# Kernel tuning notes

Measured on AMD Instinct MI355X. Metric: run time of the kernel, lower is better.

The kernel has to match this reference:

```python
import jax, jax.numpy as jnp
import numpy as np

B, T, D, H = 64, 512, 1024, 1024

def setup_inputs() -> dict:
    key = jax.random.key(0)
    k1, k2, k3, k4 = jax.random.split(key, 4)
    inputs = jax.random.normal(k1, (B, T, D), dtype=jnp.float32)
    lengths = jax.random.randint(k2, (B,), 1, T + 1, dtype=jnp.int32)
    init_c = jnp.zeros((B, H), dtype=jnp.float32)
    init_h = jnp.zeros((B, H), dtype=jnp.float32)
    # LSTMCell params: input kernel (no bias), hidden kernel + bias, gates [i,f,g,o]
    Wi = jax.random.normal(k3, (D, 4 * H), dtype=jnp.float32) / np.sqrt(D)
    Wh = jax.random.normal(k4, (H, 4 * H), dtype=jnp.float32) / np.sqrt(H)
    b = jnp.zeros((4 * H,), dtype=jnp.float32)
    return {"inputs": inputs, "lengths": lengths, "init_c": init_c,
            "init_h": init_h, "Wi": Wi, "Wh": Wh, "b": b}

def reference(inputs, lengths, init_c, init_h, Wi, Wh, b):
    # Precompute the input-side projection for all timesteps (same math as
    # per-step dense_i in flax LSTMCell, just batched).
    x_proj = jnp.einsum('btd,dg->btg', inputs, Wi) + b  # [B, T, 4H]

    def step(carry, x):
        c, h = carry
        z = x + h @ Wh  # [B, 4H]
        i, f, g, o = jnp.split(z, 4, axis=-1)
        i = jax.nn.sigmoid(i)
        f = jax.nn.sigmoid(f)
        g = jnp.tanh(g)
        o = jax.nn.sigmoid(o)
        new_c = f * c + i * g
        new_h = o * jnp.tanh(new_c)
        return (new_c, new_h), (new_c, new_h)

    _, (cs, hs) = jax.lax.scan(step, (init_c, init_h),
                               jnp.swapaxes(x_proj, 0, 1))  # [T, B, H] each
    outputs = jnp.swapaxes(hs, 0, 1)       # [B, T, H]
    cell_cs = jnp.swapaxes(cs, 0, 1)       # [B, T, H]
    idx = jnp.arange(inputs.shape[0])
    final_c = cell_cs[idx, lengths - 1]    # [B, H]
    final_h = outputs[idx, lengths - 1]    # [B, H]
    return outputs, final_c, final_h
```

## Files before the change

### kernel.cpp

```cpp
#include <hip/hip_runtime.h>

#define B_ 64
#define T_ 512
#define D_ 1024
#define H_ 1024

typedef _Float16 half8 __attribute__((ext_vector_type(8)));
typedef float floatx16 __attribute__((ext_vector_type(16)));

__device__ __forceinline__ float sigm(float x)   { return 1.f / (1.f + __expf(-x)); }
__device__ __forceinline__ float tanh_f(float x) { return 1.f - 2.f / (1.f + __expf(2.f * x)); }

__global__ void k_prep_x(const float* __restrict__ x, _Float16* __restrict__ xf) {
  int i = blockIdx.x * blockDim.x + threadIdx.x;
  const float4* p = (const float4*)x + (size_t)i * 2;
  float4 a = p[0], b = p[1];
  half8 v;
  v[0]=(_Float16)a.x; v[1]=(_Float16)a.y; v[2]=(_Float16)a.z; v[3]=(_Float16)a.w;
  v[4]=(_Float16)b.x; v[5]=(_Float16)b.y; v[6]=(_Float16)b.z; v[7]=(_Float16)b.w;
  ((half8*)xf)[i] = v;
}

__global__ void k_prep_misc(const float* __restrict__ init_h,
                            _Float16* __restrict__ hb1, int* __restrict__ flags) {
  int i = blockIdx.x * blockDim.x + threadIdx.x;
  hb1[i] = (_Float16)init_h[i];
  if (i < 4096) flags[i] = 0;
}

template <bool XF16>
__launch_bounds__(256, 1)
__global__ void k_lstm(const float* __restrict__ x32, const _Float16* __restrict__ xf,
                       const int* __restrict__ lengths, const float* __restrict__ init_c,
                       const float* __restrict__ Wi, const float* __restrict__ Wh,
                       const float* __restrict__ bias,
                       _Float16* __restrict__ hb0, _Float16* __restrict__ hb1,
                       int* __restrict__ flags,
                       float* __restrict__ out, float* __restrict__ finc,
                       float* __restrict__ finh)
{
  __shared__ _Float16 slab[32768];
  __shared__ _Float16 hlds[32][1028];
  __shared__ float red[4][32][40];

  const int w    = blockIdx.x;
  const int bh   = w >> 7;
  const int jc   = w & 127;
  const int t    = threadIdx.x;
  const int wave = t >> 6;
  const int lane = t & 63;
  const int m    = lane & 31;
  const int kh   = lane >> 5;

  const int gate = m >> 3;
  const int col  = gate * H_ + jc * 8 + (m & 7);

  for (int kbb = 0; kbb < 16; ++kbb) {
    const int kb = kbb * 4 + wave;
    const int kc = kb * 16 + kh * 8;
    half8 v;
    #pragma unroll
    for (int j = 0; j < 8; ++j)
      v[j] = (_Float16)Wh[(size_t)(kc + j) * 4096 + col];
    *(half8*)&slab[kb * 512 + lane * 8] = v;
  }

  half8 wia[16];
  #pragma unroll
  for (int i = 0; i < 16; ++i) {
    const int kc = (wave * 16 + i) * 16 + kh * 8;
    half8 v;
    #pragma unroll
    for (int j = 0; j < 8; ++j)
      v[j] = (_Float16)Wi[(size_t)(kc + j) * 4096 + col];
    wia[i] = v;
  }

  const int bl = t >> 3, jj = t & 7;
  const int bG = bh * 32 + bl;
  const int jG = jc * 8 + jj;
  float c = init_c[bG * H_ + jG];
  const int len = lengths[bG];
  const float bz0 = bias[0 * H_ + jG];
  const float bz1 = bias[1 * H_ + jG];
  const float bz2 = bias[2 * H_ + jG];
  const float bz3 = bias[3 * H_ + jG];

  const int bA = bh * 32 + m;
  const _Float16* xbase   = XF16 ? (xf + (size_t)bA * T_ * D_ + kh * 8) : (const _Float16*)0;
  const float*    xbase32 = x32 + (size_t)bA * T_ * D_ + kh * 8;

  int* myflag_w = flags + (w << 4);
  int* pollflag = flags + ((bh * 128 + wave * 32 + m) << 4);

  __syncthreads();

  half8 xa[16];
  if (XF16) {
    const _Float16* xs = xbase;
    #pragma unroll
    for (int i = 0; i < 16; ++i)
      xa[i] = *(const half8*)(xs + (wave * 16 + i) * 16);
  }

  for (int s = 0; s < T_; ++s) {
    if (lane < 32) {
      int spin = 0;
      while (__hip_atomic_load(pollflag, __ATOMIC_RELAXED, __HIP_MEMORY_SCOPE_AGENT) < s) {
        __builtin_amdgcn_s_sleep(1);
        if (++spin > (1 << 22)) break;
      }
    }

    const _Float16* hsrc = (s & 1) ? hb0 : hb1;
    const unsigned long long* hq =
        (const unsigned long long*)hsrc + (size_t)bh * 8192;
    unsigned long long q[32];
    #pragma unroll
    for (int r = 0; r < 32; ++r)
      q[r] = __hip_atomic_load(hq + r * 256 + wave * 64 + lane,
                               __ATOMIC_RELAXED, __HIP_MEMORY_SCOPE_AGENT);

    floatx16 C;
    #pragma unroll
    for (int r = 0; r < 16; ++r) C[r] = 0.f;
    if (XF16) {
      #pragma unroll
      for (int i = 0; i < 16; ++i)
        C = __builtin_amdgcn_mfma_f32_32x32x16_f16(xa[i], wia[i], C, 0, 0, 0);
    } else {
      const float* xs = xbase32 + (size_t)s * D_;
      #pragma unroll
      for (int i = 0; i < 16; ++i) {
        const float4* p = (const float4*)(xs + (wave * 16 + i) * 16);
        float4 u0 = p[0], u1 = p[1];
        half8 v;
        v[0]=(_Float16)u0.x; v[1]=(_Float16)u0.y; v[2]=(_Float16)u0.z; v[3]=(_Float16)u0.w;
        v[4]=(_Float16)u1.x; v[5]=(_Float16)u1.y; v[6]=(_Float16)u1.z; v[7]=(_Float16)u1.w;
        C = __builtin_amdgcn_mfma_f32_32x32x16_f16(v, wia[i], C, 0, 0, 0);
      }
    }

    #pragma unroll
    for (int r = 0; r < 32; ++r)
      *(unsigned long long*)&hlds[r][wave * 256 + lane * 4] = q[r];

    #pragma unroll
    for (int i = 0; i < 16; ++i) {
      const half8 av = *(const half8*)&hlds[m][wave * 256 + i * 16 + kh * 8];
      const half8 bf = *(const half8*)&slab[(wave * 16 + i) * 512 + lane * 8];
      C = __builtin_amdgcn_mfma_f32_32x32x16_f16(av, bf, C, 0, 0, 0);
    }

    #pragma unroll
    for (int r = 0; r < 16; ++r) {
      const int row = (r & 3) + 8 * (r >> 2) + 4 * kh;
      red[wave][row][m] = C[r];
    }
    __syncthreads();

    const float z0 = red[0][bl][jj]      + red[1][bl][jj]      + red[2][bl][jj]      + red[3][bl][jj]      + bz0;
    const float z1 = red[0][bl][8 + jj]  + red[1][bl][8 + jj]  + red[2][bl][8 + jj]  + red[3][bl][8 + jj]  + bz1;
    const float z2 = red[0][bl][16 + jj] + red[1][bl][16 + jj] + red[2][bl][16 + jj] + red[3][bl][16 + jj] + bz2;
    const float z3 = red[0][bl][24 + jj] + red[1][bl][24 + jj] + red[2][bl][24 + jj] + red[3][bl][24 + jj] + bz3;

    const float ig = sigm(z0);
    const float fg = sigm(z1);
    const float gg = tanh_f(z2);
    const float og = sigm(z3);
    c = fg * c + ig * gg;
    const float hv = og * tanh_f(c);

    {
      const float hv_other = __shfl_xor(hv, 1);
      if (!(t & 1)) {
        union { _Float16 h2[2]; unsigned u; } pk;
        pk.h2[0] = (_Float16)hv;
        pk.h2[1] = (_Float16)hv_other;
        _Float16* hdst = (s & 1) ? hb1 : hb0;
        __hip_atomic_store((unsigned*)(hdst + (size_t)bG * H_ + jG), pk.u,
                           __ATOMIC_RELAXED, __HIP_MEMORY_SCOPE_AGENT);
      }
    }

    __syncthreads();
    if (t == 0)
      __hip_atomic_store(myflag_w, s + 1, __ATOMIC_RELAXED, __HIP_MEMORY_SCOPE_AGENT);

    __builtin_nontemporal_store(hv, &out[((size_t)bG * T_ + s) * H_ + jG]);
    if (s == len - 1) {
      __builtin_nontemporal_store(c,  &finc[bG * H_ + jG]);
      __builtin_nontemporal_store(hv, &finh[bG * H_ + jG]);
    }

    if (XF16 && (s + 1 < T_)) {
      const _Float16* xs = xbase + (size_t)(s + 1) * D_;
      #pragma unroll
      for (int i = 0; i < 16; ++i)
        xa[i] = *(const half8*)(xs + (wave * 16 + i) * 16);
    }
  }
}

extern "C" void kernel_launch(void* const* d_in, const int* in_sizes, int n_in,
                              void* d_out, int out_size, void* d_ws, size_t ws_size,
                              hipStream_t stream) {
  const float* x32    = (const float*)d_in[0];
  const int*   lens   = (const int*)  d_in[1];
  const float* init_c = (const float*)d_in[2];
  const float* init_h = (const float*)d_in[3];
  const float* Wi     = (const float*)d_in[4];
  const float* Wh     = (const float*)d_in[5];
  const float* bias   = (const float*)d_in[6];

  float* out   = (float*)d_out;
  float* fin_c = out + (size_t)B_ * T_ * H_;
  float* fin_h = fin_c + (size_t)B_ * H_;

  char* ws = (char*)d_ws;
  int*       flags = (int*)ws;
  _Float16*  hb0   = (_Float16*)(ws + 16384);
  _Float16*  hb1   = hb0 + (size_t)B_ * H_;
  _Float16*  xf16  = (_Float16*)(ws + (1u << 20));

  const size_t need_big = (1u << 20) + sizeof(_Float16) * (size_t)B_ * T_ * D_;

  k_prep_misc<<<256, 256, 0, stream>>>(init_h, hb1, flags);
  if (ws_size >= need_big) {
    k_prep_x<<<16384, 256, 0, stream>>>(x32, xf16);
    k_lstm<true><<<256, 256, 0, stream>>>(x32, xf16, lens, init_c, Wi, Wh, bias,
                                          hb0, hb1, flags, out, fin_c, fin_h);
  } else {
    k_lstm<false><<<256, 256, 0, stream>>>(x32, xf16, lens, init_c, Wi, Wh, bias,
                                           hb0, hb1, flags, out, fin_c, fin_h);
  }
}
```

Measured before the change: 2.471 ms.

## Replace per-step flag polling with epoch bits embedded in fp16 hidden data

```diff
diff --git a/kernel.cpp b/kernel.cpp
--- a/kernel.cpp
+++ b/kernel.cpp
@@ -22,10 +22,13 @@
 }
 
 __global__ void k_prep_misc(const float* __restrict__ init_h,
-                            _Float16* __restrict__ hb1, int* __restrict__ flags) {
+                            unsigned short* __restrict__ hb0,
+                            unsigned short* __restrict__ hb1) {
   int i = blockIdx.x * blockDim.x + threadIdx.x;
-  hb1[i] = (_Float16)init_h[i];
-  if (i < 4096) flags[i] = 0;
+  union { _Float16 h; unsigned short u; } cv;
+  cv.h = (_Float16)init_h[i];
+  hb1[i] = (unsigned short)~cv.u;
+  hb0[i] = 0xFFFFu;
 }
 
 template <bool XF16>
@@ -35,7 +38,6 @@
                        const float* __restrict__ Wi, const float* __restrict__ Wh,
                        const float* __restrict__ bias,
                        _Float16* __restrict__ hb0, _Float16* __restrict__ hb1,
-                       int* __restrict__ flags,
                        float* __restrict__ out, float* __restrict__ finc,
                        float* __restrict__ finh)
 {
@@ -90,9 +92,6 @@
   const _Float16* xbase   = XF16 ? (xf + (size_t)bA * T_ * D_ + kh * 8) : (const _Float16*)0;
   const float*    xbase32 = x32 + (size_t)bA * T_ * D_ + kh * 8;
 
-  int* myflag_w = flags + (w << 4);
-  int* pollflag = flags + ((bh * 128 + wave * 32 + m) << 4);
-
   __syncthreads();
 
   half8 xa[16];
@@ -104,17 +103,11 @@
   }
 
   for (int s = 0; s < T_; ++s) {
-    if (lane < 32) {
-      int spin = 0;
-      while (__hip_atomic_load(pollflag, __ATOMIC_RELAXED, __HIP_MEMORY_SCOPE_AGENT) < s) {
-        __builtin_amdgcn_s_sleep(1);
-        if (++spin > (1 << 22)) break;
-      }
-    }
+    const int eg = (s == 0) ? 1 : (((s - 1) >> 1) & 1);
 
     const _Float16* hsrc = (s & 1) ? hb0 : hb1;
-    const unsigned long long* hq =
-        (const unsigned long long*)hsrc + (size_t)bh * 8192;
+    unsigned long long* hq =
+        (unsigned long long*)hsrc + (size_t)bh * 8192;
     unsigned long long q[32];
     #pragma unroll
     for (int r = 0; r < 32; ++r)
@@ -141,6 +134,28 @@
       }
     }
 
+    {
+      int spin = 0;
+      while (true) {
+        bool all = true;
+        #pragma unroll
+        for (int r = 0; r < 32; ++r) {
+          if ((int)((q[r] >> 14) & 1ull) != eg) {
+            q[r] = __hip_atomic_load(hq + r * 256 + wave * 64 + lane,
+                                     __ATOMIC_RELAXED, __HIP_MEMORY_SCOPE_AGENT);
+            all = false;
+          }
+        }
+        if (all) break;
+        __builtin_amdgcn_s_sleep(1);
+        if (++spin > (1 << 21)) break;
+      }
+      if (eg) {
+        #pragma unroll
+        for (int r = 0; r < 32; ++r) q[r] = ~q[r];
+      }
+    }
+
     #pragma unroll
     for (int r = 0; r < 32; ++r)
       *(unsigned long long*)&hlds[r][wave * 256 + lane * 4] = q[r];
@@ -151,6 +166,8 @@
       const half8 bf = *(const half8*)&slab[(wave * 16 + i) * 512 + lane * 8];
       C = __builtin_amdgcn_mfma_f32_32x32x16_f16(av, bf, C, 0, 0, 0);
     }
+
+    __syncthreads();
 
     #pragma unroll
     for (int r = 0; r < 16; ++r) {
@@ -172,20 +189,20 @@
     const float hv = og * tanh_f(c);
 
     {
-      const float hv_other = __shfl_xor(hv, 1);
-      if (!(t & 1)) {
-        union { _Float16 h2[2]; unsigned u; } pk;
-        pk.h2[0] = (_Float16)hv;
-        pk.h2[1] = (_Float16)hv_other;
+      const int g = (s >> 1) & 1;
+      union { _Float16 h2[2]; unsigned u; } pk;
+      pk.h2[0] = (_Float16)hv;
+      pk.h2[1] = (_Float16)__shfl_xor(hv, 1);
+      const unsigned other = __shfl_xor(pk.u, 2);
+      if ((t & 3) == 0) {
+        unsigned long long qq = (unsigned long long)pk.u
+                              | ((unsigned long long)other << 32);
+        if (g) qq = ~qq;
         _Float16* hdst = (s & 1) ? hb1 : hb0;
-        __hip_atomic_store((unsigned*)(hdst + (size_t)bG * H_ + jG), pk.u,
+        __hip_atomic_store((unsigned long long*)(hdst + (size_t)bG * H_ + jG), qq,
                            __ATOMIC_RELAXED, __HIP_MEMORY_SCOPE_AGENT);
       }
     }
-
-    __syncthreads();
-    if (t == 0)
-      __hip_atomic_store(myflag_w, s + 1, __ATOMIC_RELAXED, __HIP_MEMORY_SCOPE_AGENT);
 
     __builtin_nontemporal_store(hv, &out[((size_t)bG * T_ + s) * H_ + jG]);
     if (s == len - 1) {
@@ -218,20 +235,20 @@
   float* fin_h = fin_c + (size_t)B_ * H_;
 
   char* ws = (char*)d_ws;
-  int*       flags = (int*)ws;
   _Float16*  hb0   = (_Float16*)(ws + 16384);
   _Float16*  hb1   = hb0 + (size_t)B_ * H_;
   _Float16*  xf16  = (_Float16*)(ws + (1u << 20));
 
   const size_t need_big = (1u << 20) + sizeof(_Float16) * (size_t)B_ * T_ * D_;
 
-  k_prep_misc<<<256, 256, 0, stream>>>(init_h, hb1, flags);
+  k_prep_misc<<<256, 256, 0, stream>>>(init_h, (unsigned short*)hb0,
+                                       (unsigned short*)hb1);
   if (ws_size >= need_big) {
     k_prep_x<<<16384, 256, 0, stream>>>(x32, xf16);
     k_lstm<true><<<256, 256, 0, stream>>>(x32, xf16, lens, init_c, Wi, Wh, bias,
-                                          hb0, hb1, flags, out, fin_c, fin_h);
+                                          hb0, hb1, out, fin_c, fin_h);
   } else {
     k_lstm<false><<<256, 256, 0, stream>>>(x32, xf16, lens, init_c, Wi, Wh, bias,
-                                           hb0, hb1, flags, out, fin_c, fin_h);
-  }
-}
+                                           hb0, hb1, out, fin_c, fin_h);
+  }
+}
```

Result: slower. 2.889 ms (+16.9%).
